# Kernel tuning notes

Hardware: AMD Instinct MI355X
Metric: run time of the kernel (lower is better)

Reference implementation:

```python
import jax, jax.numpy as jnp
import numpy as np

N_NODES = 100000


def _gcn_layer(x, src, dst, ew, norm_s, norm_d, W, b):
    # DGL GraphConv with edge weights, norm='both':
    # h_v = D_in(v)^-1/2 * sum_{(u,v) in E} w_uv * D_out(u)^-1/2 * x_u; then Linear.
    m = (x * norm_s[:, None])[src] * ew[:, None]        # [E, d] gather + weight
    agg = jax.ops.segment_sum(m, dst, num_segments=N_NODES)  # [N, d] scatter-add
    return (agg * norm_d[:, None]) @ W + b


def setup_inputs() -> dict:
    key = jax.random.key(0)
    ks = jax.random.split(key, 12)
    N, E, D, C = N_NODES, 1600000, 64, 32
    inp = {
        "x": jax.random.normal(ks[0], (N, D), jnp.float32),
        "src": jax.random.randint(ks[1], (E,), 0, N, jnp.int64),
        "dst": jax.random.randint(ks[2], (E,), 0, N, jnp.int64),
        "ew": jax.random.uniform(ks[3], (E,), jnp.float32),
    }
    s = 1.0 / np.sqrt(D)
    for i, k in zip(range(1, 5), ks[4:8]):
        inp[f"W{i}"] = jax.random.normal(k, (D, D), jnp.float32) * s
        inp[f"b{i}"] = jnp.zeros((D,), jnp.float32)
    inp["Wr"] = jax.random.normal(ks[8], (D, D), jnp.float32) * s
    inp["br"] = jnp.zeros((D,), jnp.float32)
    inp["Wo"] = jax.random.normal(ks[9], (D, C), jnp.float32) * s
    inp["bo"] = jnp.zeros((C,), jnp.float32)
    return inp


def reference(x, src, dst, ew, W1, b1, W2, b2, W3, b3, W4, b4, Wr, br, Wo, bo):
    ones = jnp.ones(src.shape, x.dtype)
    deg_out = jnp.clip(jax.ops.segment_sum(ones, src, num_segments=N_NODES), 1.0)
    deg_in = jnp.clip(jax.ops.segment_sum(ones, dst, num_segments=N_NODES), 1.0)
    norm_s = deg_out ** -0.5
    norm_d = deg_in ** -0.5

    res = x @ Wr + br
    h = jax.nn.relu(_gcn_layer(x, src, dst, ew, norm_s, norm_d, W1, b1))
    h = jax.nn.relu(_gcn_layer(h, src, dst, ew, norm_s, norm_d, W2, b2))
    h = jax.nn.relu(_gcn_layer(h, src, dst, ew, norm_s, norm_d, W3, b3))
    h = _gcn_layer(h, src, dst, ew, norm_s, norm_d, W4, b4)
    h = jax.nn.relu(h + res)
    return h @ Wo + bo
```

## Files before the change

kernel.cpp:

```cpp
#include <hip/hip_runtime.h>

#define NN 100000
#define D 64
#define G 3
#define RS 33334
#define NC 85
#define NB (G*NC)

typedef short bf16x8 __attribute__((ext_vector_type(8)));
typedef float f32x4 __attribute__((ext_vector_type(4)));
typedef float f32x2 __attribute__((ext_vector_type(2)));

__device__ __forceinline__ float bf2f_lo(unsigned w) { return __uint_as_float(w << 16); }
__device__ __forceinline__ float bf2f_hi(unsigned w) { return __uint_as_float(w & 0xffff0000u); }
__device__ __forceinline__ unsigned short f2bf(float f) {
    unsigned u = __float_as_uint(f);
    return (unsigned short)((u + 0x7fffu + ((u >> 16) & 1u)) >> 16);
}
__device__ __forceinline__ unsigned pack2(float a, float b) {
    return (unsigned)f2bf(a) | ((unsigned)f2bf(b) << 16);
}
__device__ __forceinline__ unsigned char f2fp8(float v) {
    return (unsigned char)(__builtin_amdgcn_cvt_pk_fp8_f32(v, v, 0, false) & 0xff);
}
__device__ __forceinline__ unsigned pack_cw(int s, float w) {
    return ((unsigned)f2bf(w) << 17) | (unsigned)s;
}

__global__ __launch_bounds__(1024) void k_hist(const int* __restrict__ src,
                                               const int* __restrict__ dst,
                                               unsigned short* __restrict__ psd, int E) {
    __shared__ unsigned h[RS / 2];
    int b = blockIdx.x, t = threadIdx.x;
    int g = b / NC, c = b - g * NC;
    int lo = g * RS;
    for (int i = t; i < RS / 2; i += 1024) h[i] = 0;
    __syncthreads();
    int e0 = (int)((((long long)c * E / NC)) & ~3LL);
    int e1 = (c == NC - 1) ? E : (int)((((long long)(c + 1) * E / NC)) & ~3LL);
    int m = (e1 - e0) & ~4095;
    for (int e = e0 + t * 4; e < e0 + m; e += 4096) {
        int4 s4 = *(const int4*)(src + e);
        int4 d4 = *(const int4*)(dst + e);
        int v;
        v = s4.x - lo; if ((unsigned)v < RS) atomicAdd(&h[v >> 1], 1u << ((v & 1) * 16));
        v = s4.y - lo; if ((unsigned)v < RS) atomicAdd(&h[v >> 1], 1u << ((v & 1) * 16));
        v = s4.z - lo; if ((unsigned)v < RS) atomicAdd(&h[v >> 1], 1u << ((v & 1) * 16));
        v = s4.w - lo; if ((unsigned)v < RS) atomicAdd(&h[v >> 1], 1u << ((v & 1) * 16));
        v = d4.x - lo; if ((unsigned)v < RS) atomicAdd(&h[v >> 1], 1u << ((v & 1) * 16 + 8));
        v = d4.y - lo; if ((unsigned)v < RS) atomicAdd(&h[v >> 1], 1u << ((v & 1) * 16 + 8));
        v = d4.z - lo; if ((unsigned)v < RS) atomicAdd(&h[v >> 1], 1u << ((v & 1) * 16 + 8));
        v = d4.w - lo; if ((unsigned)v < RS) atomicAdd(&h[v >> 1], 1u << ((v & 1) * 16 + 8));
    }
    for (int e = e0 + m + t; e < e1; e += 1024) {
        int v = src[e] - lo; if ((unsigned)v < RS) atomicAdd(&h[v >> 1], 1u << ((v & 1) * 16));
        v = dst[e] - lo;     if ((unsigned)v < RS) atomicAdd(&h[v >> 1], 1u << ((v & 1) * 16 + 8));
    }
    __syncthreads();
    unsigned* pb = (unsigned*)(psd + (size_t)b * RS);
    for (int i = t; i < RS / 2; i += 1024) pb[i] = h[i];
}

__global__ __launch_bounds__(1024) void k_scan1m(const unsigned short* __restrict__ psd,
                                                 float* __restrict__ ns, float* __restrict__ nd,
                                                 int* __restrict__ rowptr,
                                                 int* __restrict__ bsum, int n) {
    __shared__ int lds[1024];
    int t = threadIdx.x;
    int i = blockIdx.x * 1024 + t;
    int sv = 0, dv = 0;
    if (i < n) {
        int g = i / RS, off = i - g * RS;
        const unsigned short* p = psd + (size_t)(g * NC) * RS + off;
        #pragma unroll 5
        for (int c = 0; c < NC; ++c) {
            unsigned v = p[(size_t)c * RS];
            sv += (int)(v & 0xffu);
            dv += (int)(v >> 8);
        }
        ns[i] = rsqrtf(fmaxf((float)sv, 1.0f));
        nd[i] = rsqrtf(fmaxf((float)dv, 1.0f));
    }
    lds[t] = dv;
    __syncthreads();
    for (int off = 1; off < 1024; off <<= 1) {
        int v = lds[t];
        int a = (t >= off) ? lds[t - off] : 0;
        __syncthreads();
        lds[t] = v + a;
        __syncthreads();
    }
    if (t == 1023) bsum[blockIdx.x] = lds[1023];
    if (i < n) rowptr[i] = lds[t] - dv;
}

__global__ void k_scan3c(int* __restrict__ rowptr, const int* __restrict__ bsum,
                         const unsigned short* __restrict__ psd,
                         unsigned short* __restrict__ cur16,
                         int n, int E, int nb) {
    __shared__ int sbs[128];
    int t = threadIdx.x;
    if (t < 128) sbs[t] = (t < nb) ? bsum[t] : 0;
    __syncthreads();
    for (int off = 1; off < 128; off <<= 1) {
        int v = 0, a = 0;
        if (t < 128) { v = sbs[t]; if (t >= off) a = sbs[t - off]; }
        __syncthreads();
        if (t < 128) sbs[t] = v + a;
        __syncthreads();
    }
    int i = blockIdx.x * blockDim.x + t;
    if (i == 0) rowptr[n] = E;
    if (i >= n) return;
    int blk = i >> 10;
    int base = (blk > 0) ? sbs[blk - 1] : 0;
    int r = rowptr[i] + base;
    rowptr[i] = r;
    int g = i / RS, off = i - g * RS;
    const unsigned short* p = psd + (size_t)(g * NC) * RS + off;
    unsigned short* cp = cur16 + (size_t)(g * NC) * RS + off;
    int run = 0;
    #pragma unroll 5
    for (int c = 0; c < NC; ++c) {
        cp[(size_t)c * RS] = (unsigned short)run;
        run += (int)(p[(size_t)c * RS] >> 8);
    }
}

__global__ __launch_bounds__(1024) void k_fillsort(const int* __restrict__ src,
                                                   const int* __restrict__ dst,
                                                   const float* __restrict__ ew,
                                                   const int* __restrict__ rowptr,
                                                   const unsigned short* __restrict__ cur16,
                                                   unsigned* __restrict__ cw, int E) {
    __shared__ int cur[RS];
    int b = blockIdx.x, t = threadIdx.x;
    int g = b / NC, c = b - g * NC;
    int lo = g * RS;
    const unsigned short* c16 = cur16 + (size_t)b * RS;
    for (int i = t; i < RS; i += 1024) cur[i] = rowptr[lo + i] + (int)c16[i];
    __syncthreads();
    int e0 = (int)((((long long)c * E / NC)) & ~3LL);
    int e1 = (c == NC - 1) ? E : (int)((((long long)(c + 1) * E / NC)) & ~3LL);
    int m = (e1 - e0) & ~4095;
    for (int e = e0 + t * 4; e < e0 + m; e += 4096) {
        int4 s4 = *(const int4*)(src + e);
        int4 d4 = *(const int4*)(dst + e);
        float4 w4 = *(const float4*)(ew + e);
        int d;
        d = d4.x - lo; if ((unsigned)d < RS) { int p = atomicAdd(&cur[d], 1); cw[p] = pack_cw(s4.x, w4.x); }
        d = d4.y - lo; if ((unsigned)d < RS) { int p = atomicAdd(&cur[d], 1); cw[p] = pack_cw(s4.y, w4.y); }
        d = d4.z - lo; if ((unsigned)d < RS) { int p = atomicAdd(&cur[d], 1); cw[p] = pack_cw(s4.z, w4.z); }
        d = d4.w - lo; if ((unsigned)d < RS) { int p = atomicAdd(&cur[d], 1); cw[p] = pack_cw(s4.w, w4.w); }
    }
    for (int e = e0 + m + t; e < e1; e += 1024) {
        int d = dst[e] - lo;
        if ((unsigned)d < RS) {
            int p = atomicAdd(&cur[d], 1);
            cw[p] = pack_cw(src[e], ew[e]);
        }
    }
}

__global__ __launch_bounds__(256) void k_gemm2(const float* __restrict__ x,
                                               const float* __restrict__ Wr,
                                               const float* __restrict__ brs,
                                               const float* __restrict__ W1,
                                               const float* __restrict__ ns,
                                               unsigned short* __restrict__ resb,
                                               unsigned char* __restrict__ tmat, int n) {
    __shared__ unsigned short WTr[64][72];
    __shared__ unsigned short WT1[64][72];
    int t = threadIdx.x;
    for (int i = t; i < 64 * 64; i += 256) {
        int k = i >> 6, nn = i & 63;
        WTr[nn][k] = f2bf(Wr[i]);
        WT1[nn][k] = f2bf(W1[i]);
    }
    __syncthreads();
    int w = t >> 6, lane = t & 63;
    int m = lane & 15, q = lane >> 4;
    int node0 = blockIdx.x * 64 + w * 16;
    int nodeA = min(node0 + m, n - 1);
    const float* inf = x + (size_t)nodeA * D;
    float sc = ns[nodeA];
    bf16x8 afr[2], afs[2];
    #pragma unroll
    for (int kc = 0; kc < 2; ++kc) {
        float4 f0 = *(const float4*)(inf + kc * 32 + q * 8);
        float4 f1 = *(const float4*)(inf + kc * 32 + q * 8 + 4);
        union { bf16x8 v; unsigned short u[8]; } ta, ts;
        ta.u[0] = f2bf(f0.x); ta.u[1] = f2bf(f0.y);
        ta.u[2] = f2bf(f0.z); ta.u[3] = f2bf(f0.w);
        ta.u[4] = f2bf(f1.x); ta.u[5] = f2bf(f1.y);
        ta.u[6] = f2bf(f1.z); ta.u[7] = f2bf(f1.w);
        ts.u[0] = f2bf(f0.x * sc); ts.u[1] = f2bf(f0.y * sc);
        ts.u[2] = f2bf(f0.z * sc); ts.u[3] = f2bf(f0.w * sc);
        ts.u[4] = f2bf(f1.x * sc); ts.u[5] = f2bf(f1.y * sc);
        ts.u[6] = f2bf(f1.z * sc); ts.u[7] = f2bf(f1.w * sc);
        afr[kc] = ta.v;
        afs[kc] = ts.v;
    }
    #pragma unroll
    for (int nt = 0; nt < 4; ++nt) {
        f32x4 ar = {0.f, 0.f, 0.f, 0.f};
        f32x4 at = {0.f, 0.f, 0.f, 0.f};
        #pragma unroll
        for (int kc = 0; kc < 2; ++kc) {
            union { bf16x8 v; uint4 u; } bfr, bf1;
            bfr.u = *(const uint4*)&WTr[nt * 16 + m][kc * 32 + q * 8];
            bf1.u = *(const uint4*)&WT1[nt * 16 + m][kc * 32 + q * 8];
            ar = __builtin_amdgcn_mfma_f32_16x16x32_bf16(afr[kc], bfr.v, ar, 0, 0, 0);
            at = __builtin_amdgcn_mfma_f32_16x16x32_bf16(afs[kc], bf1.v, at, 0, 0, 0);
        }
        int col = nt * 16 + m;
        float bb = brs[col];
        #pragma unroll
        for (int r = 0; r < 4; ++r) {
            int node = node0 + q * 4 + r;
            if (node < n) {
                resb[(size_t)node * D + col] = f2bf(ar[r] + bb);
                tmat[(size_t)node * D + col] = f2fp8(at[r]);
            }
        }
    }
}

template<bool LAST>
__global__ void k_gather(const int* __restrict__ rowptr, const unsigned* __restrict__ cw,
                         const unsigned char* __restrict__ tmat,
                         const float* __restrict__ nd, const float* __restrict__ ns,
                         const float* __restrict__ bias,
                         const unsigned short* __restrict__ resb,
                         unsigned short* __restrict__ outb, int n, int E) {
    int node = blockIdx.x * (blockDim.x >> 5) + (threadIdx.x >> 5);
    int lane = threadIdx.x & 31;
    if (node >= n) return;
    int g = lane >> 3;
    int h = lane & 7;
    int beg = rowptr[node], end = rowptr[node + 1];
    float a0=0,a1=0,a2=0,a3=0,a4=0,a5=0,a6=0,a7=0;
    float c0=0,c1=0,c2=0,c3=0,c4=0,c5=0,c6=0,c7=0;
    for (int base = beg; base < end; base += 16) {
        int eA = base + g;
        int eB = eA + 4;
        int eC = eA + 8;
        int eD = eA + 12;
        unsigned cvA = cw[min(eA, E - 1)];
        unsigned cvB = cw[min(eB, E - 1)];
        unsigned cvC = cw[min(eC, E - 1)];
        unsigned cvD = cw[min(eD, E - 1)];
        float wA = (eA < end) ? __uint_as_float((cvA >> 17) << 16) : 0.f;
        float wB = (eB < end) ? __uint_as_float((cvB >> 17) << 16) : 0.f;
        float wC = (eC < end) ? __uint_as_float((cvC >> 17) << 16) : 0.f;
        float wD = (eD < end) ? __uint_as_float((cvD >> 17) << 16) : 0.f;
        uint2 rA = *((const uint2*)(tmat + (size_t)(cvA & 0x1FFFFu) * D) + h);
        uint2 rB = *((const uint2*)(tmat + (size_t)(cvB & 0x1FFFFu) * D) + h);
        uint2 rC = *((const uint2*)(tmat + (size_t)(cvC & 0x1FFFFu) * D) + h);
        uint2 rD = *((const uint2*)(tmat + (size_t)(cvD & 0x1FFFFu) * D) + h);
        f32x2 p0, p1, p2, p3;
        p0 = __builtin_amdgcn_cvt_pk_f32_fp8(rA.x, false);
        p1 = __builtin_amdgcn_cvt_pk_f32_fp8(rA.x, true);
        p2 = __builtin_amdgcn_cvt_pk_f32_fp8(rA.y, false);
        p3 = __builtin_amdgcn_cvt_pk_f32_fp8(rA.y, true);
        a0 += wA * p0.x; a1 += wA * p0.y; a2 += wA * p1.x; a3 += wA * p1.y;
        a4 += wA * p2.x; a5 += wA * p2.y; a6 += wA * p3.x; a7 += wA * p3.y;
        p0 = __builtin_amdgcn_cvt_pk_f32_fp8(rB.x, false);
        p1 = __builtin_amdgcn_cvt_pk_f32_fp8(rB.x, true);
        p2 = __builtin_amdgcn_cvt_pk_f32_fp8(rB.y, false);
        p3 = __builtin_amdgcn_cvt_pk_f32_fp8(rB.y, true);
        c0 += wB * p0.x; c1 += wB * p0.y; c2 += wB * p1.x; c3 += wB * p1.y;
        c4 += wB * p2.x; c5 += wB * p2.y; c6 += wB * p3.x; c7 += wB * p3.y;
        p0 = __builtin_amdgcn_cvt_pk_f32_fp8(rC.x, false);
        p1 = __builtin_amdgcn_cvt_pk_f32_fp8(rC.x, true);
        p2 = __builtin_amdgcn_cvt_pk_f32_fp8(rC.y, false);
        p3 = __builtin_amdgcn_cvt_pk_f32_fp8(rC.y, true);
        a0 += wC * p0.x; a1 += wC * p0.y; a2 += wC * p1.x; a3 += wC * p1.y;
        a4 += wC * p2.x; a5 += wC * p2.y; a6 += wC * p3.x; a7 += wC * p3.y;
        p0 = __builtin_amdgcn_cvt_pk_f32_fp8(rD.x, false);
        p1 = __builtin_amdgcn_cvt_pk_f32_fp8(rD.x, true);
        p2 = __builtin_amdgcn_cvt_pk_f32_fp8(rD.y, false);
        p3 = __builtin_amdgcn_cvt_pk_f32_fp8(rD.y, true);
        c0 += wD * p0.x; c1 += wD * p0.y; c2 += wD * p1.x; c3 += wD * p1.y;
        c4 += wD * p2.x; c5 += wD * p2.y; c6 += wD * p3.x; c7 += wD * p3.y;
    }
    a0 += c0; a1 += c1; a2 += c2; a3 += c3;
    a4 += c4; a5 += c5; a6 += c6; a7 += c7;
    #pragma unroll
    for (int msk = 8; msk <= 16; msk <<= 1) {
        a0 += __shfl_xor(a0, msk); a1 += __shfl_xor(a1, msk);
        a2 += __shfl_xor(a2, msk); a3 += __shfl_xor(a3, msk);
        a4 += __shfl_xor(a4, msk); a5 += __shfl_xor(a5, msk);
        a6 += __shfl_xor(a6, msk); a7 += __shfl_xor(a7, msk);
    }
    float ndv = nd[node];
    float4 b0 = *(const float4*)(bias + 8 * h);
    float4 b1 = *(const float4*)(bias + 8 * h + 4);
    float v0 = ndv * a0 + b0.x, v1 = ndv * a1 + b0.y;
    float v2 = ndv * a2 + b0.z, v3 = ndv * a3 + b0.w;
    float v4 = ndv * a4 + b1.x, v5 = ndv * a5 + b1.y;
    float v6 = ndv * a6 + b1.z, v7 = ndv * a7 + b1.w;
    if (LAST) {
        uint4 r = *((const uint4*)(resb + (size_t)node * D) + h);
        v0 += bf2f_lo(r.x); v1 += bf2f_hi(r.x);
        v2 += bf2f_lo(r.y); v3 += bf2f_hi(r.y);
        v4 += bf2f_lo(r.z); v5 += bf2f_hi(r.z);
        v6 += bf2f_lo(r.w); v7 += bf2f_hi(r.w);
    }
    v0 = fmaxf(v0, 0.f); v1 = fmaxf(v1, 0.f); v2 = fmaxf(v2, 0.f); v3 = fmaxf(v3, 0.f);
    v4 = fmaxf(v4, 0.f); v5 = fmaxf(v5, 0.f); v6 = fmaxf(v6, 0.f); v7 = fmaxf(v7, 0.f);
    if (!LAST) {
        float s = ns[node];
        v0 *= s; v1 *= s; v2 *= s; v3 *= s; v4 *= s; v5 *= s; v6 *= s; v7 *= s;
    }
    if (g == 0) {
        uint4 o = make_uint4(pack2(v0, v1), pack2(v2, v3), pack2(v4, v5), pack2(v6, v7));
        *((uint4*)(outb + (size_t)node * D) + h) = o;
    }
}

template<int OUTD, bool BIAS, int OUTMODE>
__global__ __launch_bounds__(256) void k_gemm(const unsigned short* __restrict__ inb,
                                              const float* __restrict__ W,
                                              const float* __restrict__ bias,
                                              void* __restrict__ out_, int n) {
    constexpr int NT = OUTD / 16;
    __shared__ unsigned short WT[OUTD][72];
    int t = threadIdx.x;
    for (int i = t; i < 64 * OUTD; i += 256) {
        int k = i / OUTD, nn = i % OUTD;
        WT[nn][k] = f2bf(W[i]);
    }
    __syncthreads();
    int w = t >> 6, lane = t & 63;
    int m = lane & 15, q = lane >> 4;
    int node0 = blockIdx.x * 64 + w * 16;
    int nodeA = min(node0 + m, n - 1);
    const unsigned short* ip = inb + (size_t)nodeA * D;
    bf16x8 afr[2];
    #pragma unroll
    for (int kc = 0; kc < 2; ++kc) {
        union { bf16x8 v; uint4 u; } tmp;
        tmp.u = *(const uint4*)(ip + kc * 32 + q * 8);
        afr[kc] = tmp.v;
    }
    #pragma unroll
    for (int nt = 0; nt < NT; ++nt) {
        f32x4 acc = {0.f, 0.f, 0.f, 0.f};
        #pragma unroll
        for (int kc = 0; kc < 2; ++kc) {
            union { bf16x8 v; uint4 u; } bfr;
            bfr.u = *(const uint4*)&WT[nt * 16 + m][kc * 32 + q * 8];
            acc = __builtin_amdgcn_mfma_f32_16x16x32_bf16(afr[kc], bfr.v, acc, 0, 0, 0);
        }
        int col = nt * 16 + m;
        float bb = BIAS ? bias[col] : 0.f;
        #pragma unroll
        for (int r = 0; r < 4; ++r) {
            int node = node0 + q * 4 + r;
            if (node < n) {
                float v = acc[r] + bb;
                if (OUTMODE == 2)
                    ((unsigned char*)out_)[(size_t)node * OUTD + col] = f2fp8(v);
                else
                    ((float*)out_)[(size_t)node * OUTD + col] = v;
            }
        }
    }
}

static inline char* align_up(char* p, size_t a) {
    return (char*)(((uintptr_t)p + a - 1) & ~(uintptr_t)(a - 1));
}

extern "C" void kernel_launch(void* const* d_in, const int* in_sizes, int n_in,
                              void* d_out, int out_size, void* d_ws, size_t ws_size,
                              hipStream_t stream) {
    const float* x   = (const float*)d_in[0];
    const int*   src = (const int*)d_in[1];
    const int*   dst = (const int*)d_in[2];
    const float* ew  = (const float*)d_in[3];
    const float* Wl[4] = {(const float*)d_in[4], (const float*)d_in[6],
                          (const float*)d_in[8], (const float*)d_in[10]};
    const float* bl[4] = {(const float*)d_in[5], (const float*)d_in[7],
                          (const float*)d_in[9], (const float*)d_in[11]};
    const float* Wr = (const float*)d_in[12];
    const float* br = (const float*)d_in[13];
    const float* Wo = (const float*)d_in[14];
    const float* bo = (const float*)d_in[15];
    float* out = (float*)d_out;

    const int N = NN;
    const int E = in_sizes[1];

    char* p = (char*)d_ws;
    float* norm_s = (float*)p;            p = align_up(p + N * 4, 256);
    float* norm_d = (float*)p;            p = align_up(p + N * 4, 256);
    int*   rowptr = (int*)p;              p = align_up(p + (size_t)(G * RS + 80) * 4, 256);
    int*   bsum   = (int*)p;              p = align_up(p + 128 * 4, 256);
    unsigned* cw  = (unsigned*)p;         p = align_up(p + (size_t)E * 4, 256);
    unsigned short* psd   = (unsigned short*)p; p = align_up(p + (size_t)NB * RS * 2, 256);
    unsigned short* cur16 = (unsigned short*)p; p = align_up(p + (size_t)NB * RS * 2, 256);
    unsigned short* resb  = (unsigned short*)p; p = align_up(p + (size_t)N * D * 2, 256);
    unsigned short* xs   = psd;
    unsigned char*  tmat = (unsigned char*)(xs + (size_t)N * D);

    k_hist<<<NB, 1024, 0, stream>>>(src, dst, psd, E);
    int nb = (N + 1023) / 1024;
    k_scan1m<<<nb, 1024, 0, stream>>>(psd, norm_s, norm_d, rowptr, bsum, N);
    k_scan3c<<<(N + 255) / 256, 256, 0, stream>>>(rowptr, bsum, psd, cur16, N, E, nb);
    k_fillsort<<<NB, 1024, 0, stream>>>(src, dst, ew, rowptr, cur16, cw, E);

    k_gemm2<<<(N + 63) / 64, 256, 0, stream>>>(x, Wr, br, Wl[0], norm_s, resb, tmat, N);

    k_gather<false><<<(N + 7) / 8, 256, 0, stream>>>(
        rowptr, cw, tmat, norm_d, norm_s, bl[0], nullptr, xs, N, E);
    k_gemm<64, false, 2><<<(N + 63) / 64, 256, 0, stream>>>(xs, Wl[1], nullptr, tmat, N);
    k_gather<false><<<(N + 7) / 8, 256, 0, stream>>>(
        rowptr, cw, tmat, norm_d, norm_s, bl[1], nullptr, xs, N, E);
    k_gemm<64, false, 2><<<(N + 63) / 64, 256, 0, stream>>>(xs, Wl[2], nullptr, tmat, N);
    k_gather<false><<<(N + 7) / 8, 256, 0, stream>>>(
        rowptr, cw, tmat, norm_d, norm_s, bl[2], nullptr, xs, N, E);
    k_gemm<64, false, 2><<<(N + 63) / 64, 256, 0, stream>>>(xs, Wl[3], nullptr, tmat, N);
    k_gather<true><<<(N + 7) / 8, 256, 0, stream>>>(
        rowptr, cw, tmat, norm_d, nullptr, bl[3], resb, xs, N, E);
    k_gemm<32, true, 0><<<(N + 63) / 64, 256, 0, stream>>>(xs, Wo, bo, out, N);
}
```

Measured before the change: 329.7 us.

## Replace LDS-partitioned histogram and fill with global atomic degree count and fill

Drops the partitioned shared-memory histogram scheme, which had every block scan its edge chunk once per node range, along with the per-chunk cursor arrays. Degrees are now counted with global atomics in a single pass over the edges, and CSR fill uses a global atomic cursor per destination. This removes the repeated edge reads and the large per-chunk cursor traffic, at the cost of global atomic contention and less coalesced writes. Edge order inside each row becomes nondeterministic in both versions.

```diff
diff --git a/kernel.cpp b/kernel.cpp
--- a/kernel.cpp
+++ b/kernel.cpp
@@ -2,10 +2,6 @@
 
 #define NN 100000
 #define D 64
-#define G 3
-#define RS 33334
-#define NC 85
-#define NB (G*NC)
 
 typedef short bf16x8 __attribute__((ext_vector_type(8)));
 typedef float f32x4 __attribute__((ext_vector_type(4)));
@@ -27,57 +23,39 @@
     return ((unsigned)f2bf(w) << 17) | (unsigned)s;
 }
 
-__global__ __launch_bounds__(1024) void k_hist(const int* __restrict__ src,
-                                               const int* __restrict__ dst,
-                                               unsigned short* __restrict__ psd, int E) {
-    __shared__ unsigned h[RS / 2];
-    int b = blockIdx.x, t = threadIdx.x;
-    int g = b / NC, c = b - g * NC;
-    int lo = g * RS;
-    for (int i = t; i < RS / 2; i += 1024) h[i] = 0;
-    __syncthreads();
-    int e0 = (int)((((long long)c * E / NC)) & ~3LL);
-    int e1 = (c == NC - 1) ? E : (int)((((long long)(c + 1) * E / NC)) & ~3LL);
-    int m = (e1 - e0) & ~4095;
-    for (int e = e0 + t * 4; e < e0 + m; e += 4096) {
-        int4 s4 = *(const int4*)(src + e);
-        int4 d4 = *(const int4*)(dst + e);
-        int v;
-        v = s4.x - lo; if ((unsigned)v < RS) atomicAdd(&h[v >> 1], 1u << ((v & 1) * 16));
-        v = s4.y - lo; if ((unsigned)v < RS) atomicAdd(&h[v >> 1], 1u << ((v & 1) * 16));
-        v = s4.z - lo; if ((unsigned)v < RS) atomicAdd(&h[v >> 1], 1u << ((v & 1) * 16));
-        v = s4.w - lo; if ((unsigned)v < RS) atomicAdd(&h[v >> 1], 1u << ((v & 1) * 16));
-        v = d4.x - lo; if ((unsigned)v < RS) atomicAdd(&h[v >> 1], 1u << ((v & 1) * 16 + 8));
-        v = d4.y - lo; if ((unsigned)v < RS) atomicAdd(&h[v >> 1], 1u << ((v & 1) * 16 + 8));
-        v = d4.z - lo; if ((unsigned)v < RS) atomicAdd(&h[v >> 1], 1u << ((v & 1) * 16 + 8));
-        v = d4.w - lo; if ((unsigned)v < RS) atomicAdd(&h[v >> 1], 1u << ((v & 1) * 16 + 8));
-    }
-    for (int e = e0 + m + t; e < e1; e += 1024) {
-        int v = src[e] - lo; if ((unsigned)v < RS) atomicAdd(&h[v >> 1], 1u << ((v & 1) * 16));
-        v = dst[e] - lo;     if ((unsigned)v < RS) atomicAdd(&h[v >> 1], 1u << ((v & 1) * 16 + 8));
-    }
-    __syncthreads();
-    unsigned* pb = (unsigned*)(psd + (size_t)b * RS);
-    for (int i = t; i < RS / 2; i += 1024) pb[i] = h[i];
-}
-
-__global__ __launch_bounds__(1024) void k_scan1m(const unsigned short* __restrict__ psd,
-                                                 float* __restrict__ ns, float* __restrict__ nd,
-                                                 int* __restrict__ rowptr,
-                                                 int* __restrict__ bsum, int n) {
+__global__ __launch_bounds__(1024) void k_deg(const int* __restrict__ src,
+                                              const int* __restrict__ dst,
+                                              int* __restrict__ degs,
+                                              int* __restrict__ degd, int E) {
+    int t = blockIdx.x * 1024 + threadIdx.x;
+    int m = E >> 2;
+    int stride = gridDim.x * 1024;
+    for (int i = t; i < m; i += stride) {
+        int4 s4 = ((const int4*)src)[i];
+        int4 d4 = ((const int4*)dst)[i];
+        atomicAdd(&degs[s4.x], 1); atomicAdd(&degs[s4.y], 1);
+        atomicAdd(&degs[s4.z], 1); atomicAdd(&degs[s4.w], 1);
+        atomicAdd(&degd[d4.x], 1); atomicAdd(&degd[d4.y], 1);
+        atomicAdd(&degd[d4.z], 1); atomicAdd(&degd[d4.w], 1);
+    }
+    for (int e = (m << 2) + t; e < E; e += stride) {
+        atomicAdd(&degs[src[e]], 1);
+        atomicAdd(&degd[dst[e]], 1);
+    }
+}
+
+__global__ __launch_bounds__(1024) void k_scanA(const int* __restrict__ degs,
+                                                const int* __restrict__ degd,
+                                                float* __restrict__ ns, float* __restrict__ nd,
+                                                int* __restrict__ rowptr,
+                                                int* __restrict__ bsum, int n) {
     __shared__ int lds[1024];
     int t = threadIdx.x;
     int i = blockIdx.x * 1024 + t;
-    int sv = 0, dv = 0;
+    int dv = 0;
     if (i < n) {
-        int g = i / RS, off = i - g * RS;
-        const unsigned short* p = psd + (size_t)(g * NC) * RS + off;
-        #pragma unroll 5
-        for (int c = 0; c < NC; ++c) {
-            unsigned v = p[(size_t)c * RS];
-            sv += (int)(v & 0xffu);
-            dv += (int)(v >> 8);
-        }
+        int sv = degs[i];
+        dv = degd[i];
         ns[i] = rsqrtf(fmaxf((float)sv, 1.0f));
         nd[i] = rsqrtf(fmaxf((float)dv, 1.0f));
     }
@@ -94,10 +72,8 @@
     if (i < n) rowptr[i] = lds[t] - dv;
 }
 
-__global__ void k_scan3c(int* __restrict__ rowptr, const int* __restrict__ bsum,
-                         const unsigned short* __restrict__ psd,
-                         unsigned short* __restrict__ cur16,
-                         int n, int E, int nb) {
+__global__ void k_scanB(int* __restrict__ rowptr, const int* __restrict__ bsum,
+                        int* __restrict__ gcur, int n, int E, int nb) {
     __shared__ int sbs[128];
     int t = threadIdx.x;
     if (t < 128) sbs[t] = (t < nb) ? bsum[t] : 0;
@@ -116,49 +92,30 @@
     int base = (blk > 0) ? sbs[blk - 1] : 0;
     int r = rowptr[i] + base;
     rowptr[i] = r;
-    int g = i / RS, off = i - g * RS;
-    const unsigned short* p = psd + (size_t)(g * NC) * RS + off;
-    unsigned short* cp = cur16 + (size_t)(g * NC) * RS + off;
-    int run = 0;
-    #pragma unroll 5
-    for (int c = 0; c < NC; ++c) {
-        cp[(size_t)c * RS] = (unsigned short)run;
-        run += (int)(p[(size_t)c * RS] >> 8);
-    }
-}
-
-__global__ __launch_bounds__(1024) void k_fillsort(const int* __restrict__ src,
-                                                   const int* __restrict__ dst,
-                                                   const float* __restrict__ ew,
-                                                   const int* __restrict__ rowptr,
-                                                   const unsigned short* __restrict__ cur16,
-                                                   unsigned* __restrict__ cw, int E) {
-    __shared__ int cur[RS];
-    int b = blockIdx.x, t = threadIdx.x;
-    int g = b / NC, c = b - g * NC;
-    int lo = g * RS;
-    const unsigned short* c16 = cur16 + (size_t)b * RS;
-    for (int i = t; i < RS; i += 1024) cur[i] = rowptr[lo + i] + (int)c16[i];
-    __syncthreads();
-    int e0 = (int)((((long long)c * E / NC)) & ~3LL);
-    int e1 = (c == NC - 1) ? E : (int)((((long long)(c + 1) * E / NC)) & ~3LL);
-    int m = (e1 - e0) & ~4095;
-    for (int e = e0 + t * 4; e < e0 + m; e += 4096) {
-        int4 s4 = *(const int4*)(src + e);
-        int4 d4 = *(const int4*)(dst + e);
-        float4 w4 = *(const float4*)(ew + e);
-        int d;
-        d = d4.x - lo; if ((unsigned)d < RS) { int p = atomicAdd(&cur[d], 1); cw[p] = pack_cw(s4.x, w4.x); }
-        d = d4.y - lo; if ((unsigned)d < RS) { int p = atomicAdd(&cur[d], 1); cw[p] = pack_cw(s4.y, w4.y); }
-        d = d4.z - lo; if ((unsigned)d < RS) { int p = atomicAdd(&cur[d], 1); cw[p] = pack_cw(s4.z, w4.z); }
-        d = d4.w - lo; if ((unsigned)d < RS) { int p = atomicAdd(&cur[d], 1); cw[p] = pack_cw(s4.w, w4.w); }
-    }
-    for (int e = e0 + m + t; e < e1; e += 1024) {
-        int d = dst[e] - lo;
-        if ((unsigned)d < RS) {
-            int p = atomicAdd(&cur[d], 1);
-            cw[p] = pack_cw(src[e], ew[e]);
-        }
+    gcur[i] = r;
+}
+
+__global__ __launch_bounds__(1024) void k_fill(const int* __restrict__ src,
+                                               const int* __restrict__ dst,
+                                               const float* __restrict__ ew,
+                                               int* __restrict__ gcur,
+                                               unsigned* __restrict__ cw, int E) {
+    int t = blockIdx.x * 1024 + threadIdx.x;
+    int m = E >> 2;
+    int stride = gridDim.x * 1024;
+    for (int i = t; i < m; i += stride) {
+        int4 s4 = ((const int4*)src)[i];
+        int4 d4 = ((const int4*)dst)[i];
+        float4 w4 = ((const float4*)ew)[i];
+        int p;
+        p = atomicAdd(&gcur[d4.x], 1); cw[p] = pack_cw(s4.x, w4.x);
+        p = atomicAdd(&gcur[d4.y], 1); cw[p] = pack_cw(s4.y, w4.y);
+        p = atomicAdd(&gcur[d4.z], 1); cw[p] = pack_cw(s4.z, w4.z);
+        p = atomicAdd(&gcur[d4.w], 1); cw[p] = pack_cw(s4.w, w4.w);
+    }
+    for (int e = (m << 2) + t; e < E; e += stride) {
+        int p = atomicAdd(&gcur[dst[e]], 1);
+        cw[p] = pack_cw(src[e], ew[e]);
     }
 }
 
@@ -396,20 +353,23 @@
     char* p = (char*)d_ws;
     float* norm_s = (float*)p;            p = align_up(p + N * 4, 256);
     float* norm_d = (float*)p;            p = align_up(p + N * 4, 256);
-    int*   rowptr = (int*)p;              p = align_up(p + (size_t)(G * RS + 80) * 4, 256);
+    int*   rowptr = (int*)p;              p = align_up(p + (size_t)(N + 64) * 4, 256);
     int*   bsum   = (int*)p;              p = align_up(p + 128 * 4, 256);
+    int*   degs   = (int*)p;
+    int*   degd   = degs + N;             p = align_up(p + (size_t)2 * N * 4, 256);
+    int*   gcur   = (int*)p;              p = align_up(p + (size_t)N * 4, 256);
     unsigned* cw  = (unsigned*)p;         p = align_up(p + (size_t)E * 4, 256);
-    unsigned short* psd   = (unsigned short*)p; p = align_up(p + (size_t)NB * RS * 2, 256);
-    unsigned short* cur16 = (unsigned short*)p; p = align_up(p + (size_t)NB * RS * 2, 256);
-    unsigned short* resb  = (unsigned short*)p; p = align_up(p + (size_t)N * D * 2, 256);
-    unsigned short* xs   = psd;
-    unsigned char*  tmat = (unsigned char*)(xs + (size_t)N * D);
-
-    k_hist<<<NB, 1024, 0, stream>>>(src, dst, psd, E);
+    unsigned short* resb = (unsigned short*)p; p = align_up(p + (size_t)N * D * 2, 256);
+    unsigned short* xs   = (unsigned short*)p; p = align_up(p + (size_t)N * D * 2, 256);
+    unsigned char*  tmat = (unsigned char*)p;  p = align_up(p + (size_t)N * D, 256);
+
+    hipMemsetAsync(degs, 0, (size_t)2 * N * 4, stream);
+    int ebl = (E / 4 + 1023) / 1024;
+    k_deg<<<ebl, 1024, 0, stream>>>(src, dst, degs, degd, E);
     int nb = (N + 1023) / 1024;
-    k_scan1m<<<nb, 1024, 0, stream>>>(psd, norm_s, norm_d, rowptr, bsum, N);
-    k_scan3c<<<(N + 255) / 256, 256, 0, stream>>>(rowptr, bsum, psd, cur16, N, E, nb);
-    k_fillsort<<<NB, 1024, 0, stream>>>(src, dst, ew, rowptr, cur16, cw, E);
+    k_scanA<<<nb, 1024, 0, stream>>>(degs, degd, norm_s, norm_d, rowptr, bsum, N);
+    k_scanB<<<(N + 255) / 256, 256, 0, stream>>>(rowptr, bsum, gcur, N, E, nb);
+    k_fill<<<ebl, 1024, 0, stream>>>(src, dst, ew, gcur, cw, E);
 
     k_gemm2<<<(N + 63) / 64, 256, 0, stream>>>(x, Wr, br, Wl[0], norm_s, resb, tmat, N);
 
```

Result: slower. 501.5 us (+52.1%).
